# Kernel tuning notes

Hardware: AMD Instinct MI355X
Metric: run time of the kernel (lower is better)

Reference implementation:

```python
import jax, jax.numpy as jnp
import numpy as np

B, T, F = 8192, 200, 16
H = 32  # LSTM units
D = 60  # 6 * FREQUENCY


def setup_inputs() -> dict:
    key = jax.random.key(0)
    ks = jax.random.split(key, 5)
    s = 0.1
    return {
        "x": jax.random.normal(ks[0], (B, T, F), jnp.float32),
        "W": jax.random.normal(ks[1], (F, 4 * H), jnp.float32) * s,
        "U": jax.random.normal(ks[2], (H, 4 * H), jnp.float32) * s,
        "b": jnp.zeros((4 * H,), jnp.float32),
        "W1": jax.random.normal(ks[3], (H, D), jnp.float32) * s,
        "b1": jnp.zeros((D,), jnp.float32),
        "W2": jax.random.normal(ks[4], (H, D), jnp.float32) * s,
        "b2": jnp.zeros((D,), jnp.float32),
    }


def _lstm_last(x, W, U, b):
    # Precompute input-to-gate projections for all timesteps: [B, T, 4H]
    xg = jnp.einsum('btf,fg->btg', x, W) + b
    batch = x.shape[0]
    h0 = jnp.zeros((batch, H), x.dtype)
    c0 = jnp.zeros((batch, H), x.dtype)

    def step(carry, xg_t):
        h, c = carry
        g = xg_t + h @ U  # [B, 4H]
        i, f, cc, o = jnp.split(g, 4, axis=-1)  # Keras gate order: i, f, c, o
        i = jax.nn.sigmoid(i)
        f = jax.nn.sigmoid(f)
        o = jax.nn.sigmoid(o)
        c_new = f * c + i * jax.nn.relu(cc)  # activation=relu
        h_new = o * jax.nn.relu(c_new)
        return (h_new, c_new), None

    (h_T, _), _ = jax.lax.scan(step, (h0, c0), jnp.swapaxes(xg, 0, 1))
    return h_T  # return_sequences=False -> last hidden state [B, H]


def reference(x, W, U, b, W1, b1, W2, b2):
    h = _lstm_last(x, W, U, b)
    long_pred = h @ W1 + b1
    lat_pred = h @ W2 + b2
    return (long_pred, lat_pred)
```

## Files before the change

### kernel.cpp

```cpp
#include <hip/hip_runtime.h>

#define BATCH 8192
#define TSTEPS 200
#define FEAT 16
#define HID 32
#define GATES 128
#define DOUT 60
#define ROWS 16
#define HSTRIDE 40

typedef __fp16 half2v __attribute__((ext_vector_type(2)));
typedef __fp16 half4v __attribute__((ext_vector_type(4)));
typedef __fp16 half8v __attribute__((ext_vector_type(8)));
typedef float  float4v __attribute__((ext_vector_type(4)));

__device__ __forceinline__ half2v pkrtz(float a, float b) {
    return __builtin_amdgcn_cvt_pkrtz(a, b);
}

__device__ __forceinline__ half4v pack4(float4 v) {
    half2v lo = pkrtz(v.x, v.y);
    half2v hi = pkrtz(v.z, v.w);
    half4v r;
    r[0] = lo[0]; r[1] = lo[1]; r[2] = hi[0]; r[3] = hi[1];
    return r;
}

__device__ __forceinline__ int gcol(int tt, int m) {
    return 32 * (tt >> 1) + 8 * (m >> 2) + (m & 3) + 4 * (tt & 1);
}

union hUn { half8v v; half2v h2[4]; };

template <bool DO_XW, bool DO_LOAD, int LOFF>
__device__ __forceinline__ void lstm_step(
    float4& XN, const float* xp,
    const half8v (&bU)[8], const half4v (&bW)[8], const float4v (&bias)[8],
    float4v (&accx)[8], hUn& hB, float (&cst)[2][4])
{
    float4v acc[8];
    #pragma unroll
    for (int tt = 0; tt < 8; tt++)
        acc[tt] = __builtin_amdgcn_mfma_f32_16x16x32_f16(
            bU[tt], hB.v, accx[tt], 0, 0, 0);

    if (DO_XW) {
        half4v ax = pack4(XN);
        #pragma unroll
        for (int tt = 0; tt < 8; tt++)
            accx[tt] = __builtin_amdgcn_mfma_f32_16x16x16f16(
                bW[tt], ax, bias[tt], 0, 0, 0);
    }
    if (DO_LOAD)
        XN = *reinterpret_cast<const float4*>(xp + LOFF);

    float ei[2][4], ef[2][4], eo[2][4];
    #pragma unroll
    for (int hf = 0; hf < 2; hf++)
        #pragma unroll
        for (int r = 0; r < 4; r++) {
            ei[hf][r] = __builtin_amdgcn_exp2f(acc[0 + hf][r]);
            ef[hf][r] = __builtin_amdgcn_exp2f(acc[2 + hf][r]);
            eo[hf][r] = __builtin_amdgcn_exp2f(acc[6 + hf][r]);
        }

    float dd[2][4], num[2][4], dov[2][4];
    #pragma unroll
    for (int hf = 0; hf < 2; hf++)
        #pragma unroll
        for (int r = 0; r < 4; r++) {
            float di = 1.0f + ei[hf][r];
            float df = 1.0f + ef[hf][r];
            dov[hf][r] = 1.0f + eo[hf][r];
            float rc = fmaxf(acc[4 + hf][r], 0.0f);
            num[hf][r] = fmaf(cst[hf][r], di, rc * df);
            dd[hf][r]  = di * df;
        }

    #pragma unroll
    for (int hf = 0; hf < 2; hf++)
        #pragma unroll
        for (int p = 0; p < 2; p++) {
            const int r0 = 2 * p, r1 = 2 * p + 1;
            float Q  = __builtin_amdgcn_rcpf(dd[hf][r0] * dd[hf][r1]);
            float c0 = num[hf][r0] * (dd[hf][r1] * Q);
            float c1 = num[hf][r1] * (dd[hf][r0] * Q);
            cst[hf][r0] = c0;
            cst[hf][r1] = c1;
            float Qo = __builtin_amdgcn_rcpf(dov[hf][r0] * dov[hf][r1]);
            float h0 = fmaxf(c0, 0.0f) * (dov[hf][r1] * Qo);
            float h1 = fmaxf(c1, 0.0f) * (dov[hf][r0] * Qo);
            hB.h2[2 * hf + p] = pkrtz(h0, h1);
        }
}

__global__ __launch_bounds__(64, 1) void lstm_mfma(
    const float* __restrict__ x,
    const float* __restrict__ W,
    const float* __restrict__ U,
    const float* __restrict__ bg,
    const float* __restrict__ W1,
    const float* __restrict__ b1,
    const float* __restrict__ W2,
    const float* __restrict__ b2,
    float* __restrict__ out)
{
    const int lane = threadIdx.x;
    const int n16  = lane & 15;
    const int g    = lane >> 4;
    const int b0   = blockIdx.x * ROWS;

    __shared__ __align__(16) __fp16 hbuf[ROWS * HSTRIDE];

    half8v  bU[8];
    half4v  bW[8];
    float4v bias[8];
    #pragma unroll
    for (int tt = 0; tt < 8; tt++) {
        const float s = ((tt >> 1) == 2) ? 1.0f : -1.44269504088896340736f;
        const int colA = gcol(tt, n16);
        half8v u8;
        #pragma unroll
        for (int j = 0; j < 8; j++)
            u8[j] = (__fp16)(U[(8 * g + j) * GATES + colA] * s);
        bU[tt] = u8;
        half4v w4;
        #pragma unroll
        for (int j = 0; j < 4; j++)
            w4[j] = (__fp16)(W[(4 * g + j) * GATES + colA] * s);
        bW[tt] = w4;
        float4v bv;
        #pragma unroll
        for (int r = 0; r < 4; r++)
            bv[r] = bg[gcol(tt, 4 * g + r)] * s;
        bias[tt] = bv;
    }

    const float* xrow = x + (size_t)(b0 + n16) * TSTEPS * FEAT + 4 * g;

    float4 xf0 = *reinterpret_cast<const float4*>(xrow + FEAT);
    float4 xf1 = *reinterpret_cast<const float4*>(xrow + 2 * FEAT);

    float4v accx[8];
    {
        half4v a0 = pack4(*reinterpret_cast<const float4*>(xrow));
        #pragma unroll
        for (int tt = 0; tt < 8; tt++)
            accx[tt] = __builtin_amdgcn_mfma_f32_16x16x16f16(
                bW[tt], a0, bias[tt], 0, 0, 0);
    }

    hUn hB;
    hB.v = (half8v)(__fp16)0.f;
    float cst[2][4] = {{0.f, 0.f, 0.f, 0.f}, {0.f, 0.f, 0.f, 0.f}};

    const float* xp = xrow;
    for (int it = 0; it < (TSTEPS - 4) / 2; ++it) {
        lstm_step<true, true, 3 * FEAT>(xf0, xp, bU, bW, bias, accx, hB, cst);
        lstm_step<true, true, 4 * FEAT>(xf1, xp, bU, bW, bias, accx, hB, cst);
        xp += 2 * FEAT;
    }
    lstm_step<true, true, 3 * FEAT>(xf0, xp, bU, bW, bias, accx, hB, cst);
    lstm_step<true, false, 0>(xf1, xp, bU, bW, bias, accx, hB, cst);
    lstm_step<true, false, 0>(xf0, xp, bU, bW, bias, accx, hB, cst);
    lstm_step<false, false, 0>(xf1, xp, bU, bW, bias, accx, hB, cst);

    *reinterpret_cast<half8v*>(&hbuf[n16 * HSTRIDE + 8 * g]) = hB.v;
    __builtin_amdgcn_wave_barrier();

    for (int idx = lane; idx < ROWS * DOUT; idx += 64) {
        const int row = idx / DOUT;
        const int d   = idx - row * DOUT;
        float s1 = b1[d], s2 = b2[d];
        #pragma unroll 8
        for (int k = 0; k < HID; k++) {
            float hv = (float)hbuf[row * HSTRIDE + k];
            s1 = fmaf(hv, W1[k * DOUT + d], s1);
            s2 = fmaf(hv, W2[k * DOUT + d], s2);
        }
        out[(size_t)(b0 + row) * DOUT + d] = s1;
        out[(size_t)BATCH * DOUT + (size_t)(b0 + row) * DOUT + d] = s2;
    }
}

extern "C" void kernel_launch(void* const* d_in, const int* in_sizes, int n_in,
                              void* d_out, int out_size, void* d_ws, size_t ws_size,
                              hipStream_t stream) {
    const float* x  = (const float*)d_in[0];
    const float* W  = (const float*)d_in[1];
    const float* U  = (const float*)d_in[2];
    const float* bg = (const float*)d_in[3];
    const float* W1 = (const float*)d_in[4];
    const float* b1 = (const float*)d_in[5];
    const float* W2 = (const float*)d_in[6];
    const float* b2 = (const float*)d_in[7];
    float* out = (float*)d_out;

    dim3 grid(BATCH / ROWS);
    dim3 block(64);
    lstm_mfma<<<grid, block, 0, stream>>>(x, W, U, bg, W1, b1, W2, b2, out);
}
```

Measured before the change: 240.2 us.

## Split recurrent MFMA into two K-halves to overlap gate epilogue with matmul

Reorganizes the per-step recurrence so the hidden state is produced in two 16-wide halves. The first half's recurrent MFMAs (16x16x16) are issued while the second half's gate epilogue computes, and the gate column mapping is changed so each half maps to contiguous columns. The goal is to shorten the serial critical path per timestep, where the MFMA latency and the transcendental epilogue ran back to back. In exchange it doubles the number of MFMA instructions (K=16 instead of K=32), changes the pipeline prologue and epilogue, and raises register pressure.

```diff
diff --git a/kernel.cpp b/kernel.cpp
--- a/kernel.cpp
+++ b/kernel.cpp
@@ -27,71 +27,84 @@
 }
 
 __device__ __forceinline__ int gcol(int tt, int m) {
-    return 32 * (tt >> 1) + 8 * (m >> 2) + (m & 3) + 4 * (tt & 1);
-}
-
-union hUn { half8v v; half2v h2[4]; };
-
-template <bool DO_XW, bool DO_LOAD, int LOFF>
+    return 32 * (tt >> 1) + 16 * (tt & 1) + m;
+}
+
+union h4Un { half4v v; half2v h2[2]; };
+
+template <int HF>
+__device__ __forceinline__ void epi_half(
+    const float4v (&acc)[8], float (&cst)[2][4], h4Un& hout)
+{
+    float ei[4], ef[4], eo[4];
+    #pragma unroll
+    for (int r = 0; r < 4; r++) {
+        ei[r] = __builtin_amdgcn_exp2f(acc[0 + HF][r]);
+        ef[r] = __builtin_amdgcn_exp2f(acc[2 + HF][r]);
+        eo[r] = __builtin_amdgcn_exp2f(acc[6 + HF][r]);
+    }
+    float dd[4], num[4], dov[4];
+    #pragma unroll
+    for (int r = 0; r < 4; r++) {
+        float di = 1.0f + ei[r];
+        float df = 1.0f + ef[r];
+        dov[r] = 1.0f + eo[r];
+        float rc = fmaxf(acc[4 + HF][r], 0.0f);
+        num[r] = fmaf(cst[HF][r], di, rc * df);
+        dd[r]  = di * df;
+    }
+    #pragma unroll
+    for (int p = 0; p < 2; p++) {
+        const int r0 = 2 * p, r1 = 2 * p + 1;
+        float Q  = __builtin_amdgcn_rcpf(dd[r0] * dd[r1]);
+        float c0 = num[r0] * (dd[r1] * Q);
+        float c1 = num[r1] * (dd[r0] * Q);
+        cst[HF][r0] = c0;
+        cst[HF][r1] = c1;
+        float Qo = __builtin_amdgcn_rcpf(dov[r0] * dov[r1]);
+        float h0 = fmaxf(c0, 0.0f) * (dov[r1] * Qo);
+        float h1 = fmaxf(c1, 0.0f) * (dov[r0] * Qo);
+        hout.h2[p] = pkrtz(h0, h1);
+    }
+}
+
+template <bool DO_XW, bool DO_LOAD, int LOFF, bool DO_REC>
 __device__ __forceinline__ void lstm_step(
     float4& XN, const float* xp,
-    const half8v (&bU)[8], const half4v (&bW)[8], const float4v (&bias)[8],
-    float4v (&accx)[8], hUn& hB, float (&cst)[2][4])
+    const half4v (&aUlo)[8], const half4v (&aUhi)[8],
+    const half4v (&bW)[8], const float4v (&bias)[8],
+    float4v (&acc)[8], float4v (&axw)[8], float (&cst)[2][4])
 {
-    float4v acc[8];
-    #pragma unroll
-    for (int tt = 0; tt < 8; tt++)
-        acc[tt] = __builtin_amdgcn_mfma_f32_16x16x32_f16(
-            bU[tt], hB.v, accx[tt], 0, 0, 0);
-
+    h4Un hlo, hhi;
+    epi_half<0>(acc, cst, hlo);
+
+    float4v pacc[8];
+    if (DO_REC) {
+        #pragma unroll
+        for (int tt = 0; tt < 8; tt++)
+            pacc[tt] = __builtin_amdgcn_mfma_f32_16x16x16f16(
+                aUlo[tt], hlo.v, axw[tt], 0, 0, 0);
+    }
+
+    epi_half<1>(acc, cst, hhi);
+
+    if (DO_REC) {
+        #pragma unroll
+        for (int q = 0; q < 8; q++) {
+            const int tt = (q < 4) ? 2 * q : 2 * (q - 4) + 1;
+            acc[tt] = __builtin_amdgcn_mfma_f32_16x16x16f16(
+                aUhi[tt], hhi.v, pacc[tt], 0, 0, 0);
+        }
+    }
     if (DO_XW) {
         half4v ax = pack4(XN);
         #pragma unroll
         for (int tt = 0; tt < 8; tt++)
-            accx[tt] = __builtin_amdgcn_mfma_f32_16x16x16f16(
+            axw[tt] = __builtin_amdgcn_mfma_f32_16x16x16f16(
                 bW[tt], ax, bias[tt], 0, 0, 0);
     }
     if (DO_LOAD)
         XN = *reinterpret_cast<const float4*>(xp + LOFF);
-
-    float ei[2][4], ef[2][4], eo[2][4];
-    #pragma unroll
-    for (int hf = 0; hf < 2; hf++)
-        #pragma unroll
-        for (int r = 0; r < 4; r++) {
-            ei[hf][r] = __builtin_amdgcn_exp2f(acc[0 + hf][r]);
-            ef[hf][r] = __builtin_amdgcn_exp2f(acc[2 + hf][r]);
-            eo[hf][r] = __builtin_amdgcn_exp2f(acc[6 + hf][r]);
-        }
-
-    float dd[2][4], num[2][4], dov[2][4];
-    #pragma unroll
-    for (int hf = 0; hf < 2; hf++)
-        #pragma unroll
-        for (int r = 0; r < 4; r++) {
-            float di = 1.0f + ei[hf][r];
-            float df = 1.0f + ef[hf][r];
-            dov[hf][r] = 1.0f + eo[hf][r];
-            float rc = fmaxf(acc[4 + hf][r], 0.0f);
-            num[hf][r] = fmaf(cst[hf][r], di, rc * df);
-            dd[hf][r]  = di * df;
-        }
-
-    #pragma unroll
-    for (int hf = 0; hf < 2; hf++)
-        #pragma unroll
-        for (int p = 0; p < 2; p++) {
-            const int r0 = 2 * p, r1 = 2 * p + 1;
-            float Q  = __builtin_amdgcn_rcpf(dd[hf][r0] * dd[hf][r1]);
-            float c0 = num[hf][r0] * (dd[hf][r1] * Q);
-            float c1 = num[hf][r1] * (dd[hf][r0] * Q);
-            cst[hf][r0] = c0;
-            cst[hf][r1] = c1;
-            float Qo = __builtin_amdgcn_rcpf(dov[hf][r0] * dov[hf][r1]);
-            float h0 = fmaxf(c0, 0.0f) * (dov[hf][r1] * Qo);
-            float h1 = fmaxf(c1, 0.0f) * (dov[hf][r0] * Qo);
-            hB.h2[2 * hf + p] = pkrtz(h0, h1);
-        }
 }
 
 __global__ __launch_bounds__(64, 1) void lstm_mfma(
@@ -112,23 +125,22 @@
 
     __shared__ __align__(16) __fp16 hbuf[ROWS * HSTRIDE];
 
-    half8v  bU[8];
-    half4v  bW[8];
+    half4v  aUlo[8], aUhi[8], bW[8];
     float4v bias[8];
     #pragma unroll
     for (int tt = 0; tt < 8; tt++) {
         const float s = ((tt >> 1) == 2) ? 1.0f : -1.44269504088896340736f;
         const int colA = gcol(tt, n16);
-        half8v u8;
-        #pragma unroll
-        for (int j = 0; j < 8; j++)
-            u8[j] = (__fp16)(U[(8 * g + j) * GATES + colA] * s);
-        bU[tt] = u8;
-        half4v w4;
-        #pragma unroll
-        for (int j = 0; j < 4; j++)
-            w4[j] = (__fp16)(W[(4 * g + j) * GATES + colA] * s);
-        bW[tt] = w4;
+        half4v ulo, uhi, w4;
+        #pragma unroll
+        for (int j = 0; j < 4; j++) {
+            ulo[j] = (__fp16)(U[(4 * g + j) * GATES + colA] * s);
+            uhi[j] = (__fp16)(U[(16 + 4 * g + j) * GATES + colA] * s);
+            w4[j]  = (__fp16)(W[(4 * g + j) * GATES + colA] * s);
+        }
+        aUlo[tt] = ulo;
+        aUhi[tt] = uhi;
+        bW[tt]   = w4;
         float4v bv;
         #pragma unroll
         for (int r = 0; r < 4; r++)
@@ -138,34 +150,40 @@
 
     const float* xrow = x + (size_t)(b0 + n16) * TSTEPS * FEAT + 4 * g;
 
-    float4 xf0 = *reinterpret_cast<const float4*>(xrow + FEAT);
-    float4 xf1 = *reinterpret_cast<const float4*>(xrow + 2 * FEAT);
-
-    float4v accx[8];
+    float4v acc[8], axw[8];
     {
         half4v a0 = pack4(*reinterpret_cast<const float4*>(xrow));
-        #pragma unroll
-        for (int tt = 0; tt < 8; tt++)
-            accx[tt] = __builtin_amdgcn_mfma_f32_16x16x16f16(
+        half4v a1 = pack4(*reinterpret_cast<const float4*>(xrow + FEAT));
+        #pragma unroll
+        for (int tt = 0; tt < 8; tt++) {
+            acc[tt] = __builtin_amdgcn_mfma_f32_16x16x16f16(
                 bW[tt], a0, bias[tt], 0, 0, 0);
-    }
-
-    hUn hB;
-    hB.v = (half8v)(__fp16)0.f;
+            axw[tt] = __builtin_amdgcn_mfma_f32_16x16x16f16(
+                bW[tt], a1, bias[tt], 0, 0, 0);
+        }
+    }
+
+    float4 xf0 = *reinterpret_cast<const float4*>(xrow + 2 * FEAT);
+    float4 xf1 = *reinterpret_cast<const float4*>(xrow + 3 * FEAT);
     float cst[2][4] = {{0.f, 0.f, 0.f, 0.f}, {0.f, 0.f, 0.f, 0.f}};
 
     const float* xp = xrow;
     for (int it = 0; it < (TSTEPS - 4) / 2; ++it) {
-        lstm_step<true, true, 3 * FEAT>(xf0, xp, bU, bW, bias, accx, hB, cst);
-        lstm_step<true, true, 4 * FEAT>(xf1, xp, bU, bW, bias, accx, hB, cst);
+        lstm_step<true, true, 4 * FEAT, true>(xf0, xp, aUlo, aUhi, bW, bias,
+                                              acc, axw, cst);
+        lstm_step<true, true, 5 * FEAT, true>(xf1, xp, aUlo, aUhi, bW, bias,
+                                              acc, axw, cst);
         xp += 2 * FEAT;
     }
-    lstm_step<true, true, 3 * FEAT>(xf0, xp, bU, bW, bias, accx, hB, cst);
-    lstm_step<true, false, 0>(xf1, xp, bU, bW, bias, accx, hB, cst);
-    lstm_step<true, false, 0>(xf0, xp, bU, bW, bias, accx, hB, cst);
-    lstm_step<false, false, 0>(xf1, xp, bU, bW, bias, accx, hB, cst);
-
-    *reinterpret_cast<half8v*>(&hbuf[n16 * HSTRIDE + 8 * g]) = hB.v;
+    lstm_step<true, false, 0, true>(xf0, xp, aUlo, aUhi, bW, bias, acc, axw, cst);
+    lstm_step<true, false, 0, true>(xf1, xp, aUlo, aUhi, bW, bias, acc, axw, cst);
+    lstm_step<false, false, 0, true>(xf0, xp, aUlo, aUhi, bW, bias, acc, axw, cst);
+    h4Un hlo, hhi;
+    epi_half<0>(acc, cst, hlo);
+    epi_half<1>(acc, cst, hhi);
+
+    *reinterpret_cast<half4v*>(&hbuf[n16 * HSTRIDE + 4 * g]) = hlo.v;
+    *reinterpret_cast<half4v*>(&hbuf[n16 * HSTRIDE + 16 + 4 * g]) = hhi.v;
     __builtin_amdgcn_wave_barrier();
 
     for (int idx = lane; idx < ROWS * DOUT; idx += 64) {
```

Result: slower. 288.1 us (+19.9%).
